# Kernel tuning notes

Measured on AMD Instinct MI355X. Metric: run time of the kernel, lower is better.

## Reference

```python
import jax, jax.numpy as jnp
import numpy as np

B, S, D_IN, D_ST = 4, 4096, 1024, 1024


def setup_inputs() -> dict:
    key = jax.random.key(0)
    ks = jax.random.split(key, 7)
    s_in = 1.0 / np.sqrt(D_IN)
    s_st = 1.0 / np.sqrt(D_ST)
    return {
        "x": jax.random.normal(ks[0], (B, S, D_IN), dtype=jnp.float32),
        "gate_w": jax.random.uniform(ks[1], (D_IN, D_ST), jnp.float32, -s_in, s_in),
        "gate_b": jax.random.uniform(ks[2], (D_ST,), jnp.float32, -s_in, s_in),
        "inp_w": jax.random.uniform(ks[3], (D_IN, D_ST), jnp.float32, -s_in, s_in),
        "inp_b": jax.random.uniform(ks[4], (D_ST,), jnp.float32, -s_in, s_in),
        "out_w": jax.random.uniform(ks[5], (D_ST, D_IN), jnp.float32, -s_st, s_st),
        "out_b": jax.random.uniform(ks[6], (D_IN,), jnp.float32, -s_st, s_st),
    }


def reference(x, gate_w, gate_b, inp_w, inp_b, out_w, out_b):
    # x: [B, S, D_in]
    inp = jnp.einsum("bsd,de->bse", x, inp_w) + inp_b      # [B,S,Dst]
    gate = jax.nn.sigmoid(jnp.einsum("bsd,de->bse", x, gate_w) + gate_b)
    b_t = (1.0 - gate) * inp                               # [B,S,Dst]

    # affine recurrence h_t = gate_t * h_{t-1} + b_t via lax.scan over time
    def step(h, ab):
        a, b = ab
        h = a * h + b
        return h, h

    a_sb = jnp.swapaxes(gate, 0, 1)  # [S,B,Dst]
    b_sb = jnp.swapaxes(b_t, 0, 1)
    h0 = jnp.zeros((x.shape[0], inp.shape[-1]), dtype=x.dtype)
    _, hs = jax.lax.scan(step, h0, (a_sb, b_sb))           # [S,B,Dst]
    scan_out = jnp.swapaxes(hs, 0, 1)                      # [B,S,Dst]

    return x + jnp.einsum("bse,ed->bsd", scan_out, out_w) + out_b
```

## Files before the change

### kernel.cpp

```cpp
#include <hip/hip_runtime.h>

typedef unsigned short u16;
typedef unsigned int   u32;
typedef __bf16 bf16x8 __attribute__((ext_vector_type(8)));
typedef float  f32x4  __attribute__((ext_vector_type(4)));

#define DEVI __device__ __forceinline__

DEVI u16 f2bf(float f) {
    union { float f; u32 u; } c; c.f = f;
    u32 u = c.u;
    u32 r = (u + 0x7fffu + ((u >> 16) & 1u)) >> 16;
    return (u16)r;
}
DEVI float bf2f(u16 v) {
    union { u32 u; float f; } c; c.u = ((u32)v) << 16;
    return c.f;
}

DEVI void gload16(const void* g, void* l) {
    __builtin_amdgcn_global_load_lds(
        (const __attribute__((address_space(1))) void*)g,
        (__attribute__((address_space(3))) void*)l, 16, 0, 0);
}


#define VMW(N)  asm volatile("s_waitcnt vmcnt(" #N ")" ::: "memory")
#define BAR     __builtin_amdgcn_s_barrier()
#define SP1     __builtin_amdgcn_s_setprio(1)
#define SP0     __builtin_amdgcn_s_setprio(0)

DEVI void stage_kh(const u16* g, u16* slot, int tid) {
    const int wvb = (tid >> 6) << 9;
    const int r = tid >> 2;
    const int p = tid & 3;
    const int c = p ^ (r & 3);
    const long off = (long)r * 1024 + (c << 3);
    gload16(g + off, slot + wvb);
    gload16(g + off + (long)128 * 1024, slot + 4096 + wvb);
}

DEVI f32x4 mfma(const bf16x8& a, const bf16x8& b, const f32x4& c) {
    return __builtin_amdgcn_mfma_f32_16x16x32_bf16(a, b, c, 0, 0, 0);
}

#define TILE_COMPUTE(q0)                                                     \
    {                                                                        \
        _Pragma("unroll")                                                    \
        for (int nf = 0; nf < 4; ++nf)                                       \
            bh[nf] = *(const bf16x8*)(lds + (q0) + bbase + nf * 512);        \
        aC0 = *(const bf16x8*)(lds + (q0) + abase);                          \
        aC1 = *(const bf16x8*)(lds + (q0) + abase + 512);                    \
        aN0 = *(const bf16x8*)(lds + (q0) + abase + 1024);                   \
        aN1 = *(const bf16x8*)(lds + (q0) + abase + 1536);                   \
        SP1;                                                                 \
        _Pragma("unroll")                                                    \
        for (int nf = 0; nf < 4; ++nf) {                                     \
            acc[0][nf] = mfma(aC0, bh[nf], acc[0][nf]);                      \
            acc[1][nf] = mfma(aC1, bh[nf], acc[1][nf]);                      \
        }                                                                    \
        SP0;                                                                 \
        aC0 = *(const bf16x8*)(lds + (q0) + abase + 2048);                   \
        aC1 = *(const bf16x8*)(lds + (q0) + abase + 2560);                   \
        SP1;                                                                 \
        _Pragma("unroll")                                                    \
        for (int nf = 0; nf < 4; ++nf) {                                     \
            acc[2][nf] = mfma(aN0, bh[nf], acc[2][nf]);                      \
            acc[3][nf] = mfma(aN1, bh[nf], acc[3][nf]);                      \
        }                                                                    \
        SP0;                                                                 \
        aN0 = *(const bf16x8*)(lds + (q0) + abase + 3072);                   \
        aN1 = *(const bf16x8*)(lds + (q0) + abase + 3584);                   \
        SP1;                                                                 \
        _Pragma("unroll")                                                    \
        for (int nf = 0; nf < 4; ++nf) {                                     \
            acc[4][nf] = mfma(aC0, bh[nf], acc[4][nf]);                      \
            acc[5][nf] = mfma(aC1, bh[nf], acc[5][nf]);                      \
        }                                                                    \
        SP0;                                                                 \
        SP1;                                                                 \
        _Pragma("unroll")                                                    \
        for (int nf = 0; nf < 4; ++nf) {                                     \
            acc[6][nf] = mfma(aN0, bh[nf], acc[6][nf]);                      \
            acc[7][nf] = mfma(aN1, bh[nf], acc[7][nf]);                      \
        }                                                                    \
        SP0;                                                                 \
    }

DEVI void pipe256(const u16* Ab, const u16* Bb, u16* lds,
                  f32x4 (&acc)[8][4], int tid) {
    const int lane = tid & 63;
    const int wm = (tid >> 6) >> 2, wn = (tid >> 6) & 3;
    const int pch = ((lane >> 4) ^ (lane & 3)) << 3;
    const int abase = (wm * 128 + (lane & 15)) * 32 + pch;
    const int bbase = 8192 + (wn * 64 + (lane & 15)) * 32 + pch;

    stage_kh(Ab,      lds + 0,     tid);
    stage_kh(Bb,      lds + 8192,  tid);
    stage_kh(Ab + 32, lds + 16384, tid);
    stage_kh(Bb + 32, lds + 24576, tid);
    VMW(4); BAR;

    bf16x8 bh[4], aC0, aC1, aN0, aN1;
    int q0 = 0, q1 = 16384, q2 = 32768;

#pragma unroll 1
    for (int t = 0; t < 30; ++t) {
        stage_kh(Ab + (t + 2) * 32, lds + q2, tid);
        stage_kh(Bb + (t + 2) * 32, lds + q2 + 8192, tid);
        TILE_COMPUTE(q0);
        VMW(4); BAR;
        int tq = q0; q0 = q1; q1 = q2; q2 = tq;
    }
    TILE_COMPUTE(q0);
    VMW(0); BAR;
    TILE_COMPUTE(q1);
}


__global__ __launch_bounds__(512, 2) void k_gemm_cat8(
    const u16* __restrict__ A, const u16* __restrict__ Bcat,
    const float* __restrict__ gb, const float* __restrict__ ib,
    u32* __restrict__ ab) {
    __shared__ __align__(16) u16 lds[49152];
    const int tid = threadIdx.x, lane = tid & 63;
    const int wm = (tid >> 6) >> 2, wn = (tid >> 6) & 3;

    int fid = (int)blockIdx.y * 8 + (int)blockIdx.x;
    int swz = (fid & 7) * 64 + (fid >> 3);
    const long bn = swz & 7, bm = swz >> 3;

    f32x4 acc[8][4] = {};
    pipe256(A + bm * 256 * 1024, Bcat + bn * 256 * 1024, lds, acc, tid);

    const long rbase = bm * 256 + wm * 128;
    const int chbase = (int)bn * 128 + wn * 32;
#pragma unroll
    for (int t = 0; t < 2; ++t) {
        int ch = chbase + t * 16 + (lane & 15);
        float g0 = gb[ch], i0 = ib[ch];
#pragma unroll
        for (int m = 0; m < 8; ++m) {
            long row = rbase + m * 16 + ((lane >> 4) << 2);
#pragma unroll
            for (int i = 0; i < 4; ++i) {
                float pg = acc[m][2 * t][i] + g0;
                float pi = acc[m][2 * t + 1][i] + i0;
                float aa = 1.0f / (1.0f + __expf(-pg));
                float bb = (1.0f - aa) * pi;
                ab[(row + i) * 1024 + ch] = (u32)f2bf(aa) | ((u32)f2bf(bb) << 16);
            }
        }
    }
}


__global__ __launch_bounds__(512, 2) void k_gemm_out8(
    const u16* __restrict__ A, const u16* __restrict__ Bt,
    const float* __restrict__ xres, const float* __restrict__ ob,
    float* __restrict__ out) {
    __shared__ __align__(16) u16 lds[49152];
    const int tid = threadIdx.x, lane = tid & 63;
    const int wm = (tid >> 6) >> 2, wn = (tid >> 6) & 3;

    int fid = (int)blockIdx.y * 4 + (int)blockIdx.x;
    int swz = (fid & 7) * 32 + (fid >> 3);
    const long bn = swz & 3, bm = swz >> 2;

    f32x4 acc[8][4] = {};
    pipe256(A + bm * 256 * 1024, Bt + bn * 256 * 1024, lds, acc, tid);

    const long rbase = bm * 256 + wm * 128;
    const int cbase = (int)bn * 256 + wn * 64;
#pragma unroll
    for (int n = 0; n < 4; ++n) {
        int col = cbase + n * 16 + (lane & 15);
        float o0 = ob[col];
#pragma unroll
        for (int m = 0; m < 8; ++m) {
            long row = rbase + m * 16 + ((lane >> 4) << 2);
#pragma unroll
            for (int i = 0; i < 4; ++i) {
                long o = (row + i) * 1024 + col;
                out[o] = acc[m][n][i] + o0 + xres[o];
            }
        }
    }
}


__global__ __launch_bounds__(256) void k_cvt_x(const float4* __restrict__ x,
                                               uint2* __restrict__ o, int n4) {
    int i = blockIdx.x * 256 + threadIdx.x;
    if (i < n4) {
        float4 v = x[i];
        uint2 r;
        r.x = (u32)f2bf(v.x) | ((u32)f2bf(v.y) << 16);
        r.y = (u32)f2bf(v.z) | ((u32)f2bf(v.w) << 16);
        o[i] = r;
    }
}

__global__ __launch_bounds__(256) void k_transpose_bf(const float* __restrict__ w,
                                                      u16* __restrict__ wt, int R, int C) {
    __shared__ float t[32][33];
    int c0 = blockIdx.x * 32, r0 = blockIdx.y * 32;
    int x = threadIdx.x & 31, y = threadIdx.x >> 5;
    for (int i = y; i < 32; i += 8) t[i][x] = w[(size_t)(r0 + i) * C + c0 + x];
    __syncthreads();
    for (int i = y; i < 32; i += 8) wt[(size_t)(c0 + i) * R + r0 + x] = f2bf(t[x][i]);
}

__global__ __launch_bounds__(256) void k_transpose_cat(const float* __restrict__ gw,
                                                       const float* __restrict__ iw,
                                                       u16* __restrict__ wt, int K, int C) {
    __shared__ float t[32][33];
    int c0 = blockIdx.x * 32, r0 = blockIdx.y * 32;
    const float* w = blockIdx.z ? iw : gw;
    int x = threadIdx.x & 31, y = threadIdx.x >> 5;
    for (int i = y; i < 32; i += 8) t[i][x] = w[(size_t)(r0 + i) * C + c0 + x];
    __syncthreads();
    for (int i = y; i < 32; i += 8) {
        int ch = c0 + i;
        int r = ((ch >> 4) << 5) | ((int)blockIdx.z << 4) | (ch & 15);
        wt[(size_t)r * K + r0 + x] = f2bf(t[x][i]);
    }
}


__global__ __launch_bounds__(256) void k_scanA(const u32* __restrict__ ab,
                                               float2* __restrict__ cAB) {
    int e = blockIdx.x * 256 + threadIdx.x;
    int c = blockIdx.y, bt = blockIdx.z;
    long base = ((long)bt * 4096 + c * 64) * 1024 + e;
    float Aa = 1.f, H = 0.f;
#pragma unroll 4
    for (int i = 0; i < 64; ++i) {
        u32 v = ab[base + (long)i * 1024];
        float a = bf2f((u16)v), b = bf2f((u16)(v >> 16));
        H = a * H + b;
        Aa *= a;
    }
    cAB[((long)bt * 64 + c) * 1024 + e] = make_float2(Aa, H);
}

__global__ __launch_bounds__(256) void k_scanB(const float2* __restrict__ cAB,
                                               float* __restrict__ hin) {
    int e = blockIdx.x * 256 + threadIdx.x;
    int bt = blockIdx.y;
    float H = 0.f;
#pragma unroll
    for (int c = 0; c < 64; ++c) {
        long s = ((long)bt * 64 + c) * 1024 + e;
        hin[s] = H;
        float2 v = cAB[s];
        H = v.x * H + v.y;
    }
}

__global__ __launch_bounds__(256) void k_scanC(const u32* __restrict__ ab,
                                               const float* __restrict__ hin,
                                               u16* __restrict__ hout) {
    int e = blockIdx.x * 256 + threadIdx.x;
    int c = blockIdx.y, bt = blockIdx.z;
    long base = ((long)bt * 4096 + c * 64) * 1024 + e;
    float H = hin[((long)bt * 64 + c) * 1024 + e];
#pragma unroll 4
    for (int i = 0; i < 64; ++i) {
        u32 v = ab[base + (long)i * 1024];
        H = bf2f((u16)v) * H + bf2f((u16)(v >> 16));
        hout[base + (long)i * 1024] = f2bf(H);
    }
}


extern "C" void kernel_launch(void* const* d_in, const int* in_sizes, int n_in,
                              void* d_out, int out_size, void* d_ws, size_t ws_size,
                              hipStream_t stream) {
    const float* x      = (const float*)d_in[0];
    const float* gate_w = (const float*)d_in[1];
    const float* gate_b = (const float*)d_in[2];
    const float* inp_w  = (const float*)d_in[3];
    const float* inp_b  = (const float*)d_in[4];
    const float* out_w  = (const float*)d_in[5];
    const float* out_b  = (const float*)d_in[6];
    float* out = (float*)d_out;

    const int Bsz = 4, S = 4096, Din = 1024, Dst = 1024;
    const int M = Bsz * S;
    const long nx = (long)M * Din;

    char* w = (char*)d_ws;
    u16* xb      = (u16*)(w);
    u16* catW    = (u16*)(w + 33554432);
    u16* owT     = (u16*)(w + 37748736);
    u16* hbf     = (u16*)(w + 39845888);
    float2* cAB  = (float2*)(w + 73400320);
    float* hin   = (float*)(w + 75497472);

    u32* ab = (u32*)d_out;

    k_cvt_x<<<(int)(nx / 4 / 256), 256, 0, stream>>>((const float4*)x, (uint2*)xb, (int)(nx / 4));
    k_transpose_cat<<<dim3(Dst / 32, Din / 32, 2), 256, 0, stream>>>(gate_w, inp_w, catW, Din, Dst);
    k_transpose_bf<<<dim3(Din / 32, Dst / 32), 256, 0, stream>>>(out_w, owT, Dst, Din);

    k_gemm_cat8<<<dim3(8, M / 256), 512, 0, stream>>>(xb, catW, gate_b, inp_b, ab);

    k_scanA<<<dim3(4, 64, Bsz), 256, 0, stream>>>(ab, cAB);
    k_scanB<<<dim3(4, Bsz), 256, 0, stream>>>(cAB, hin);
    k_scanC<<<dim3(4, 64, Bsz), 256, 0, stream>>>(ab, hin, hbf);

    k_gemm_out8<<<dim3(4, M / 256), 512, 0, stream>>>(hbf, owT, x, out_b, out);
}
```

Before: 188.0 us.

## Load GEMM A operand straight into registers and keep only B in LDS

```diff
diff --git a/kernel.cpp b/kernel.cpp
--- a/kernel.cpp
+++ b/kernel.cpp
@@ -25,7 +25,7 @@
 }
 
 
-#define VMW(N)  asm volatile("s_waitcnt vmcnt(" #N ")" ::: "memory")
+#define VMW0    asm volatile("s_waitcnt vmcnt(0)" ::: "memory")
 #define BAR     __builtin_amdgcn_s_barrier()
 #define SP1     __builtin_amdgcn_s_setprio(1)
 #define SP0     __builtin_amdgcn_s_setprio(0)
@@ -44,47 +44,26 @@
     return __builtin_amdgcn_mfma_f32_16x16x32_bf16(a, b, c, 0, 0, 0);
 }
 
-#define TILE_COMPUTE(q0)                                                     \
+#define GT(QCUR, QSTG, ACUR, ANXT, TSTG, TNXT, DO_STAGE, DO_LOAD, DO_BAR)   \
     {                                                                        \
+        if (DO_STAGE) stage_kh(Bb + (TSTG) * 32, lds + (QSTG), tid);         \
+        if (DO_LOAD) {                                                       \
+            _Pragma("unroll")                                                \
+            for (int m = 0; m < 8; ++m)                                      \
+                ANXT[m] = *(const bf16x8*)(Aq + (TNXT) * 32 + m * 16384);    \
+        }                                                                    \
         _Pragma("unroll")                                                    \
         for (int nf = 0; nf < 4; ++nf)                                       \
-            bh[nf] = *(const bf16x8*)(lds + (q0) + bbase + nf * 512);        \
-        aC0 = *(const bf16x8*)(lds + (q0) + abase);                          \
-        aC1 = *(const bf16x8*)(lds + (q0) + abase + 512);                    \
-        aN0 = *(const bf16x8*)(lds + (q0) + abase + 1024);                   \
-        aN1 = *(const bf16x8*)(lds + (q0) + abase + 1536);                   \
+            bh[nf] = *(const bf16x8*)(lds + (QCUR) + bbase + nf * 512);      \
         SP1;                                                                 \
         _Pragma("unroll")                                                    \
-        for (int nf = 0; nf < 4; ++nf) {                                     \
-            acc[0][nf] = mfma(aC0, bh[nf], acc[0][nf]);                      \
-            acc[1][nf] = mfma(aC1, bh[nf], acc[1][nf]);                      \
+        for (int m = 0; m < 8; ++m) {                                        \
+            _Pragma("unroll")                                                \
+            for (int nf = 0; nf < 4; ++nf)                                   \
+                acc[m][nf] = mfma(ACUR[m], bh[nf], acc[m][nf]);              \
         }                                                                    \
         SP0;                                                                 \
-        aC0 = *(const bf16x8*)(lds + (q0) + abase + 2048);                   \
-        aC1 = *(const bf16x8*)(lds + (q0) + abase + 2560);                   \
-        SP1;                                                                 \
-        _Pragma("unroll")                                                    \
-        for (int nf = 0; nf < 4; ++nf) {                                     \
-            acc[2][nf] = mfma(aN0, bh[nf], acc[2][nf]);                      \
-            acc[3][nf] = mfma(aN1, bh[nf], acc[3][nf]);                      \
-        }                                                                    \
-        SP0;                                                                 \
-        aN0 = *(const bf16x8*)(lds + (q0) + abase + 3072);                   \
-        aN1 = *(const bf16x8*)(lds + (q0) + abase + 3584);                   \
-        SP1;                                                                 \
-        _Pragma("unroll")                                                    \
-        for (int nf = 0; nf < 4; ++nf) {                                     \
-            acc[4][nf] = mfma(aC0, bh[nf], acc[4][nf]);                      \
-            acc[5][nf] = mfma(aC1, bh[nf], acc[5][nf]);                      \
-        }                                                                    \
-        SP0;                                                                 \
-        SP1;                                                                 \
-        _Pragma("unroll")                                                    \
-        for (int nf = 0; nf < 4; ++nf) {                                     \
-            acc[6][nf] = mfma(aN0, bh[nf], acc[6][nf]);                      \
-            acc[7][nf] = mfma(aN1, bh[nf], acc[7][nf]);                      \
-        }                                                                    \
-        SP0;                                                                 \
+        if (DO_BAR) BAR;                                                     \
     }
 
 DEVI void pipe256(const u16* Ab, const u16* Bb, u16* lds,
@@ -92,29 +71,30 @@
     const int lane = tid & 63;
     const int wm = (tid >> 6) >> 2, wn = (tid >> 6) & 3;
     const int pch = ((lane >> 4) ^ (lane & 3)) << 3;
-    const int abase = (wm * 128 + (lane & 15)) * 32 + pch;
-    const int bbase = 8192 + (wn * 64 + (lane & 15)) * 32 + pch;
-
-    stage_kh(Ab,      lds + 0,     tid);
-    stage_kh(Bb,      lds + 8192,  tid);
-    stage_kh(Ab + 32, lds + 16384, tid);
-    stage_kh(Bb + 32, lds + 24576, tid);
-    VMW(4); BAR;
-
-    bf16x8 bh[4], aC0, aC1, aN0, aN1;
-    int q0 = 0, q1 = 16384, q2 = 32768;
+    const int bbase = (wn * 64 + (lane & 15)) * 32 + pch;
+    const u16* Aq = Ab + (long)(wm * 128 + (lane & 15)) * 1024 + ((lane >> 4) << 3);
+
+    bf16x8 aA[8], aB[8], bh[4];
+
+    stage_kh(Bb,      lds + 0,    tid);
+    stage_kh(Bb + 32, lds + 8192, tid);
+#pragma unroll
+    for (int m = 0; m < 8; ++m)
+        aA[m] = *(const bf16x8*)(Aq + m * 16384);
+    VMW0; BAR;
 
 #pragma unroll 1
-    for (int t = 0; t < 30; ++t) {
-        stage_kh(Ab + (t + 2) * 32, lds + q2, tid);
-        stage_kh(Bb + (t + 2) * 32, lds + q2 + 8192, tid);
-        TILE_COMPUTE(q0);
-        VMW(4); BAR;
-        int tq = q0; q0 = q1; q1 = q2; q2 = tq;
-    }
-    TILE_COMPUTE(q0);
-    VMW(0); BAR;
-    TILE_COMPUTE(q1);
+    for (int j = 0; j < 5; ++j) {
+        const int t = j * 6;
+        GT(0,     16384, aA, aB, t + 2, t + 1, 1, 1, 1);
+        GT(8192,  0,     aB, aA, t + 3, t + 2, 1, 1, 1);
+        GT(16384, 8192,  aA, aB, t + 4, t + 3, 1, 1, 1);
+        GT(0,     16384, aB, aA, t + 5, t + 4, 1, 1, 1);
+        GT(8192,  0,     aA, aB, t + 6, t + 5, 1, 1, 1);
+        GT(16384, 8192,  aB, aA, t + 7, t + 6, 1, 1, 1);
+    }
+    GT(0,    0, aA, aB, 0, 31, 0, 1, 1);
+    GT(8192, 0, aB, aA, 0, 0,  0, 0, 0);
 }
 
 
@@ -122,7 +102,7 @@
     const u16* __restrict__ A, const u16* __restrict__ Bcat,
     const float* __restrict__ gb, const float* __restrict__ ib,
     u32* __restrict__ ab) {
-    __shared__ __align__(16) u16 lds[49152];
+    __shared__ __align__(16) u16 lds[24576];
     const int tid = threadIdx.x, lane = tid & 63;
     const int wm = (tid >> 6) >> 2, wn = (tid >> 6) & 3;
 
@@ -159,7 +139,7 @@
     const u16* __restrict__ A, const u16* __restrict__ Bt,
     const float* __restrict__ xres, const float* __restrict__ ob,
     float* __restrict__ out) {
-    __shared__ __align__(16) u16 lds[49152];
+    __shared__ __align__(16) u16 lds[24576];
     const int tid = threadIdx.x, lane = tid & 63;
     const int wm = (tid >> 6) >> 2, wn = (tid >> 6) & 3;
 
```

Result: slower. 310.4 us (+65.1%).
